# Performance work log

Hardware: AMD Instinct MI355X
Metric: run time of the kernel (lower is better)

## Reference

```python
import jax, jax.numpy as jnp
import numpy as np

N = 100000      # nodes
E = 1600000     # directed edges (avg degree 16)
F_IN = 512      # config.input_layer
H1, D1 = 8, 8   # conv1: 8 heads x 8 dims
C_OUT = 40      # config.output_layer


def setup_inputs() -> dict:
    key = jax.random.key(0)
    ks = jax.random.split(key, 10)
    x = jax.random.normal(ks[0], (N, F_IN), dtype=jnp.float32)
    edge_index = jax.random.randint(ks[1], (2, E), 0, N, dtype=jnp.int64)
    s = 0.05
    W1 = jax.random.normal(ks[2], (F_IN, H1 * D1), dtype=jnp.float32) * s
    att_src1 = jax.random.normal(ks[3], (H1, D1), dtype=jnp.float32) * s
    att_dst1 = jax.random.normal(ks[4], (H1, D1), dtype=jnp.float32) * s
    b1 = jnp.zeros((H1 * D1,), dtype=jnp.float32)
    W2 = jax.random.normal(ks[5], (H1 * D1, C_OUT), dtype=jnp.float32) * s
    att_src2 = jax.random.normal(ks[6], (1, C_OUT), dtype=jnp.float32) * s
    att_dst2 = jax.random.normal(ks[7], (1, C_OUT), dtype=jnp.float32) * s
    b2 = jnp.zeros((C_OUT,), dtype=jnp.float32)
    return {"x": x, "edge_index": edge_index,
            "W1": W1, "att_src1": att_src1, "att_dst1": att_dst1, "b1": b1,
            "W2": W2, "att_src2": att_src2, "att_dst2": att_dst2, "b2": b2}


def _gat_conv(x, src, dst, W, a_src, a_dst, b, heads, concat):
    """PyG GATConv (eval mode: attention dropout is identity)."""
    n = x.shape[0]
    d = W.shape[1] // heads
    h = (x @ W).reshape(n, heads, d)                       # [N,H,D]
    alpha_s = jnp.einsum('nhd,hd->nh', h, a_src)           # [N,H]
    alpha_d = jnp.einsum('nhd,hd->nh', h, a_dst)
    e = jax.nn.leaky_relu(alpha_s[src] + alpha_d[dst], 0.2)  # [E,H]
    # numerically stable segment softmax over edges grouped by dst
    e = e - jax.ops.segment_max(e, dst, num_segments=n)[dst]
    ex = jnp.exp(e)
    denom = jax.ops.segment_sum(ex, dst, num_segments=n)[dst]
    alpha = ex / denom                                      # [E,H]
    msg = h[src] * alpha[:, :, None]                        # [E,H,D]
    out = jax.ops.segment_sum(msg, dst, num_segments=n)     # [N,H,D]
    out = out.reshape(n, heads * d) if concat else out.mean(axis=1)
    return out + b


def reference(x, edge_index, W1, att_src1, att_dst1, b1, W2, att_src2, att_dst2, b2):
    # add self loops (PyG GATConv default)
    loop = jnp.arange(x.shape[0], dtype=edge_index.dtype)
    src = jnp.concatenate([edge_index[0], loop])
    dst = jnp.concatenate([edge_index[1], loop])
    # dropout(p=0.6) layers are identity in eval mode
    h = jax.nn.elu(_gat_conv(x, src, dst, W1, att_src1, att_dst1, b1, H1, True))
    out = _gat_conv(h, src, dst, W2, att_src2, att_dst2, b2, 1, False)
    return jax.nn.log_softmax(out, axis=1)
```

## Files before the change

### kernel.cpp

```cpp
#include <hip/hip_runtime.h>

#define F_IN 512
#define H1   8
#define D1   8
#define C1   64
#define C2   40
#define C2P  48

#define BKT_SH   7
#define BKT_W    128
#define NBKT_MAX 1024
#define NBLK     128

using short8 = __attribute__((ext_vector_type(8))) short;
using f32x4  = __attribute__((ext_vector_type(4))) float;
using bf8v   = __attribute__((ext_vector_type(8))) __bf16;

__device__ __forceinline__ float leaky02(float x) { return x > 0.f ? x : 0.2f * x; }
__device__ __forceinline__ float bf2f(unsigned short u) {
    return __builtin_bit_cast(float, ((unsigned)u) << 16);
}
__device__ __forceinline__ unsigned short f2bf(float v) {
    return __builtin_bit_cast(unsigned short, (__bf16)v);
}
__device__ __forceinline__ short8 cvt_bf16x8(float4 a, float4 b) {
    bf8v r;
    r[0] = (__bf16)a.x; r[1] = (__bf16)a.y; r[2] = (__bf16)a.z; r[3] = (__bf16)a.w;
    r[4] = (__bf16)b.x; r[5] = (__bf16)b.y; r[6] = (__bf16)b.z; r[7] = (__bf16)b.w;
    return __builtin_bit_cast(short8, r);
}

__global__ __launch_bounds__(256) void wconv_kernel(
    const float* __restrict__ W1, const float* __restrict__ W2,
    unsigned short* __restrict__ Bt1, unsigned short* __restrict__ Bt2)
{
    int idx = blockIdx.x * 256 + threadIdx.x;
    if (idx < F_IN * C1) {
        int k = idx >> 6, c = idx & 63;
        Bt1[(size_t)c * F_IN + k] = f2bf(W1[idx]);
    } else if (idx < F_IN * C1 + C2P * 64) {
        int j = idx - F_IN * C1;
        int c = j >> 6, k = j & 63;
        float v = (c < C2) ? W2[k * C2 + c] : 0.f;
        Bt2[c * 64 + k] = f2bf(v);
    }
}

__global__ __launch_bounds__(256) void gemm1_kernel(
    const float* __restrict__ x, const unsigned short* __restrict__ Bt1,
    const float* __restrict__ a_src, const float* __restrict__ a_dst,
    unsigned short* __restrict__ h1b, float* __restrict__ as1,
    float* __restrict__ ad1, int N)
{
    const int tid  = threadIdx.x;
    const int w    = tid >> 6;
    const int lane = tid & 63;
    const int lo   = lane & 15;
    const int kg   = lane >> 4;
    const int n0   = blockIdx.x * 128 + w * 32;

    const int nA = min(n0 + lo, N - 1);
    const int nB = min(n0 + 16 + lo, N - 1);
    const float* xA = x + (size_t)nA * F_IN + kg * 8;
    const float* xB = x + (size_t)nB * F_IN + kg * 8;
    const unsigned short* bp = Bt1 + (size_t)lo * F_IN + kg * 8;

    float a_s[4], a_d[4];
    #pragma unroll
    for (int nt = 0; nt < 4; ++nt) {
        a_s[nt] = a_src[nt * 16 + lo];
        a_d[nt] = a_dst[nt * 16 + lo];
    }

    f32x4 acc[2][4];
    #pragma unroll
    for (int mt = 0; mt < 2; ++mt)
        #pragma unroll
        for (int nt = 0; nt < 4; ++nt)
            acc[mt][nt] = (f32x4){0.f, 0.f, 0.f, 0.f};

    #pragma unroll 4
    for (int s = 0; s < 16; ++s) {
        const int kb = s * 32;
        float4 a0 = *(const float4*)(xA + kb);
        float4 a1 = *(const float4*)(xA + kb + 4);
        float4 c0 = *(const float4*)(xB + kb);
        float4 c1 = *(const float4*)(xB + kb + 4);
        short8 bF[4];
        #pragma unroll
        for (int nt = 0; nt < 4; ++nt)
            bF[nt] = *(const short8*)(bp + (size_t)nt * 16 * F_IN + kb);
        short8 aF0 = cvt_bf16x8(a0, a1);
        short8 aF1 = cvt_bf16x8(c0, c1);
        #pragma unroll
        for (int nt = 0; nt < 4; ++nt) {
            acc[0][nt] = __builtin_amdgcn_mfma_f32_16x16x32_bf16(aF0, bF[nt], acc[0][nt], 0, 0, 0);
            acc[1][nt] = __builtin_amdgcn_mfma_f32_16x16x32_bf16(aF1, bF[nt], acc[1][nt], 0, 0, 0);
        }
    }

    #pragma unroll
    for (int mt = 0; mt < 2; ++mt) {
        #pragma unroll
        for (int j = 0; j < 4; ++j) {
            const int n = n0 + mt * 16 + kg * 4 + j;
            float sv[4], dv[4];
            #pragma unroll
            for (int nt = 0; nt < 4; ++nt) {
                float v = acc[mt][nt][j];
                sv[nt] = v * a_s[nt];
                dv[nt] = v * a_d[nt];
            }
            #pragma unroll
            for (int m = 1; m < 8; m <<= 1) {
                #pragma unroll
                for (int nt = 0; nt < 4; ++nt) {
                    sv[nt] += __shfl_xor(sv[nt], m);
                    dv[nt] += __shfl_xor(dv[nt], m);
                }
            }
            if (n < N) {
                #pragma unroll
                for (int nt = 0; nt < 4; ++nt)
                    h1b[(size_t)n * C1 + nt * 16 + lo] = f2bf(acc[mt][nt][j]);
                if ((lane & 7) == 0) {
                    const int h0 = (lane >> 3) & 1;
                    #pragma unroll
                    for (int nt = 0; nt < 4; ++nt) {
                        as1[n * H1 + h0 + nt * 2] = sv[nt];
                        ad1[n * H1 + h0 + nt * 2] = dv[nt];
                    }
                }
            }
        }
    }
}

__global__ __launch_bounds__(256) void bhist_kernel(
    const int* __restrict__ ei, int* __restrict__ blockhist,
    int E, int nbkt, int chunk)
{
    __shared__ int lh[NBKT_MAX];
    for (int i = threadIdx.x; i < nbkt; i += 256) lh[i] = 0;
    __syncthreads();
    const int b = blockIdx.x;
    const int beg = b * chunk;
    const int end = min(E, beg + chunk);
    for (int e = beg + threadIdx.x; e < end; e += 256)
        atomicAdd(&lh[ei[E + e] >> BKT_SH], 1);
    __syncthreads();
    for (int k = threadIdx.x; k < nbkt; k += 256)
        blockhist[k * NBLK + b] = lh[k];
}

__global__ __launch_bounds__(512) void scan1_kernel(
    const int* __restrict__ in, int* __restrict__ excl,
    int* __restrict__ bsum, int M)
{
    __shared__ int sA[512], sB[512];
    const int t = threadIdx.x;
    const int i = blockIdx.x * 512 + t;
    int v = (i < M) ? in[i] : 0;
    sA[t] = v; __syncthreads();
    int* pin = sA; int* pout = sB;
    #pragma unroll
    for (int off = 1; off < 512; off <<= 1) {
        pout[t] = pin[t] + ((t >= off) ? pin[t - off] : 0);
        __syncthreads();
        int* tmp = pin; pin = pout; pout = tmp;
    }
    if (i < M) excl[i] = pin[t] - v;
    if (t == 511) bsum[blockIdx.x] = pin[511];
}

__global__ __launch_bounds__(256) void scan2_kernel(
    int* __restrict__ bsum, int* __restrict__ bsumo, int NB)
{
    __shared__ int sA[256], sB[256];
    const int t = threadIdx.x;
    int v = (t < NB) ? bsum[t] : 0;
    sA[t] = v; __syncthreads();
    int* pin = sA; int* pout = sB;
    #pragma unroll
    for (int off = 1; off < 256; off <<= 1) {
        pout[t] = pin[t] + ((t >= off) ? pin[t - off] : 0);
        __syncthreads();
        int* tmp = pin; pin = pout; pout = tmp;
    }
    if (t < NB) bsumo[t] = pin[t] - v;
}

__global__ __launch_bounds__(256) void bpart_kernel(
    const int* __restrict__ ei, const int* __restrict__ boffs,
    const int* __restrict__ bsumo, int* __restrict__ ebuf,
    int E, int nbkt, int chunk)
{
    __shared__ int cur[NBKT_MAX];
    const int b = blockIdx.x;
    for (int k = threadIdx.x; k < nbkt; k += 256) {
        const int idx = k * NBLK + b;
        cur[k] = boffs[idx] + bsumo[idx >> 9];
    }
    __syncthreads();
    const int beg = b * chunk;
    const int end = min(E, beg + chunk);
    for (int e = beg + threadIdx.x; e < end; e += 256) {
        int src = ei[e], dst = ei[E + e];
        int pos = atomicAdd(&cur[dst >> BKT_SH], 1);
        ebuf[pos] = (src << BKT_SH) | (dst & (BKT_W - 1));
    }
}

__global__ __launch_bounds__(256) void bsort_kernel(
    const int* __restrict__ boffs, const int* __restrict__ bsumo,
    const int* __restrict__ ebuf, int* __restrict__ rowptr,
    int* __restrict__ esrc, int N, int E, int nbkt)
{
    const int b = blockIdx.x;
    const int tid = threadIdx.x;
    const int i0 = b * NBLK;
    const int base = boffs[i0] + bsumo[i0 >> 9];
    int nxt;
    if (b == nbkt - 1) nxt = E;
    else {
        const int i1 = (b + 1) * NBLK;
        nxt = boffs[i1] + bsumo[i1 >> 9];
    }
    const int cnt = nxt - base;

    __shared__ int hist[BKT_W], scn[BKT_W], cur[BKT_W];
    if (tid < BKT_W) hist[tid] = 0;
    __syncthreads();
    for (int i = tid; i < cnt; i += 256)
        atomicAdd(&hist[ebuf[base + i] & (BKT_W - 1)], 1);
    __syncthreads();
    if (tid < BKT_W) scn[tid] = hist[tid];
    __syncthreads();
    #pragma unroll
    for (int off = 1; off < BKT_W; off <<= 1) {
        int add = 0;
        if (tid < BKT_W && tid >= off) add = scn[tid - off];
        __syncthreads();
        if (tid < BKT_W) scn[tid] += add;
        __syncthreads();
    }
    if (tid < BKT_W) {
        int ex = base + scn[tid] - hist[tid];
        cur[tid] = ex;
        int n0 = b * BKT_W + tid;
        if (n0 < N) rowptr[n0] = ex;
    }
    if (b == 0 && tid == 0) rowptr[N] = E;
    __syncthreads();
    for (int i = tid; i < cnt; i += 256) {
        int p = ebuf[base + i];
        int pos = atomicAdd(&cur[p & (BKT_W - 1)], 1);
        esrc[pos] = (unsigned)p >> BKT_SH;
    }
}

__global__ __launch_bounds__(256) void agg1_kernel(
    const int* __restrict__ rowptr, const int* __restrict__ esrc,
    const unsigned short* __restrict__ h1b, const float* __restrict__ as1,
    const float* __restrict__ ad1, const float* __restrict__ b1,
    unsigned short* __restrict__ h1f, int N)
{
    const int n = blockIdx.x * 4 + (threadIdx.x >> 6);
    if (n >= N) return;
    const int lane = threadIdx.x & 63;
    const int h = lane >> 3;
    const float adh = ad1[n * H1 + h];

    float acc = 0.f, den = 0.f;
    int i = rowptr[n];
    const int end = rowptr[n + 1];
    int s0, s1, s2, s3;
    if (i + 4 <= end) { s0 = esrc[i]; s1 = esrc[i+1]; s2 = esrc[i+2]; s3 = esrc[i+3]; }
    for (; i + 4 <= end; ) {
        const float v0 = bf2f(h1b[(size_t)s0 * C1 + lane]);
        const float v1 = bf2f(h1b[(size_t)s1 * C1 + lane]);
        const float v2 = bf2f(h1b[(size_t)s2 * C1 + lane]);
        const float v3 = bf2f(h1b[(size_t)s3 * C1 + lane]);
        const float a0 = as1[s0 * H1 + h], a1 = as1[s1 * H1 + h];
        const float a2 = as1[s2 * H1 + h], a3 = as1[s3 * H1 + h];
        i += 4;
        const int t0 = esrc[i], t1 = esrc[i+1], t2 = esrc[i+2], t3 = esrc[i+3];
        const float e0 = __expf(leaky02(a0 + adh));
        const float e1 = __expf(leaky02(a1 + adh));
        const float e2 = __expf(leaky02(a2 + adh));
        const float e3 = __expf(leaky02(a3 + adh));
        acc += e0 * v0; acc += e1 * v1; acc += e2 * v2; acc += e3 * v3;
        den += (e0 + e1) + (e2 + e3);
        s0 = t0; s1 = t1; s2 = t2; s3 = t3;
    }
    for (; i < end; ++i) {
        const int src = esrc[i];
        const float v  = bf2f(h1b[(size_t)src * C1 + lane]);
        const float ex = __expf(leaky02(as1[src * H1 + h] + adh));
        acc += ex * v;
        den += ex;
    }
    {
        const float ex = __expf(leaky02(as1[n * H1 + h] + adh));
        acc += ex * bf2f(h1b[(size_t)n * C1 + lane]);
        den += ex;
    }
    float v = acc / den + b1[lane];
    v = v > 0.f ? v : __expf(v) - 1.f;
    h1f[(size_t)n * C1 + lane] = f2bf(v);
}

__global__ __launch_bounds__(256) void gemm2_kernel(
    const unsigned short* __restrict__ h1f, const unsigned short* __restrict__ Bt2,
    const float* __restrict__ a_src2, const float* __restrict__ a_dst2,
    unsigned short* __restrict__ h2b, float* __restrict__ as2,
    float* __restrict__ ad2, int N)
{
    const int tid  = threadIdx.x;
    const int w    = tid >> 6;
    const int lane = tid & 63;
    const int lo   = lane & 15;
    const int kg   = lane >> 4;
    const int n0   = blockIdx.x * 64 + w * 16;

    const int nA = min(n0 + lo, N - 1);
    const unsigned short* ap = h1f + (size_t)nA * C1 + kg * 8;

    float a_s[3], a_d[3];
    #pragma unroll
    for (int nt = 0; nt < 3; ++nt) {
        const int c = nt * 16 + lo;
        a_s[nt] = (c < C2) ? a_src2[c] : 0.f;
        a_d[nt] = (c < C2) ? a_dst2[c] : 0.f;
    }

    f32x4 acc[3];
    #pragma unroll
    for (int nt = 0; nt < 3; ++nt) acc[nt] = (f32x4){0.f, 0.f, 0.f, 0.f};

    #pragma unroll
    for (int ks = 0; ks < 2; ++ks) {
        short8 aF = *(const short8*)(ap + ks * 32);
        #pragma unroll
        for (int nt = 0; nt < 3; ++nt) {
            short8 bF = *(const short8*)(Bt2 + (nt * 16 + lo) * 64 + ks * 32 + kg * 8);
            acc[nt] = __builtin_amdgcn_mfma_f32_16x16x32_bf16(aF, bF, acc[nt], 0, 0, 0);
        }
    }

    #pragma unroll
    for (int j = 0; j < 4; ++j) {
        const int n = n0 + kg * 4 + j;
        float s = acc[0][j] * a_s[0] + acc[1][j] * a_s[1] + acc[2][j] * a_s[2];
        float d = acc[0][j] * a_d[0] + acc[1][j] * a_d[1] + acc[2][j] * a_d[2];
        #pragma unroll
        for (int m = 1; m < 16; m <<= 1) {
            s += __shfl_xor(s, m);
            d += __shfl_xor(d, m);
        }
        if (n < N) {
            #pragma unroll
            for (int nt = 0; nt < 3; ++nt) {
                const int c = nt * 16 + lo;
                if (c < C2) h2b[(size_t)n * C2 + c] = f2bf(acc[nt][j]);
            }
            if (lo == 0) { as2[n] = s; ad2[n] = d; }
        }
    }
}

__global__ __launch_bounds__(256) void agg2_kernel(
    const int* __restrict__ rowptr, const int* __restrict__ esrc,
    const unsigned short* __restrict__ h2b, const float* __restrict__ as2,
    const float* __restrict__ ad2, const float* __restrict__ b2,
    float* __restrict__ out, int N)
{
    const int n = blockIdx.x * 4 + (threadIdx.x >> 6);
    if (n >= N) return;
    const int lane = threadIdx.x & 63;
    const float adn = ad2[n];

    float acc = 0.f, den = 0.f;
    int i = rowptr[n];
    const int end = rowptr[n + 1];
    int s0, s1, s2, s3;
    if (i + 4 <= end) { s0 = esrc[i]; s1 = esrc[i+1]; s2 = esrc[i+2]; s3 = esrc[i+3]; }
    for (; i + 4 <= end; ) {
        float v0 = 0.f, v1 = 0.f, v2 = 0.f, v3 = 0.f;
        if (lane < C2) {
            v0 = bf2f(h2b[(size_t)s0 * C2 + lane]);
            v1 = bf2f(h2b[(size_t)s1 * C2 + lane]);
            v2 = bf2f(h2b[(size_t)s2 * C2 + lane]);
            v3 = bf2f(h2b[(size_t)s3 * C2 + lane]);
        }
        const float a0 = as2[s0], a1 = as2[s1], a2 = as2[s2], a3 = as2[s3];
        i += 4;
        const int t0 = esrc[i], t1 = esrc[i+1], t2 = esrc[i+2], t3 = esrc[i+3];
        const float e0 = __expf(leaky02(a0 + adn));
        const float e1 = __expf(leaky02(a1 + adn));
        const float e2 = __expf(leaky02(a2 + adn));
        const float e3 = __expf(leaky02(a3 + adn));
        acc += e0 * v0; acc += e1 * v1; acc += e2 * v2; acc += e3 * v3;
        den += (e0 + e1) + (e2 + e3);
        s0 = t0; s1 = t1; s2 = t2; s3 = t3;
    }
    for (; i < end; ++i) {
        const int src = esrc[i];
        float v = (lane < C2) ? bf2f(h2b[(size_t)src * C2 + lane]) : 0.f;
        const float ex = __expf(leaky02(as2[src] + adn));
        acc += ex * v;
        den += ex;
    }
    {
        const float ex = __expf(leaky02(as2[n] + adn));
        if (lane < C2) acc += ex * bf2f(h2b[(size_t)n * C2 + lane]);
        den += ex;
    }
    float v = (lane < C2) ? (acc / den + b2[lane]) : -1e30f;
    float m = v;
    #pragma unroll
    for (int s = 1; s < 64; s <<= 1) m = fmaxf(m, __shfl_xor(m, s));
    float e2x = (lane < C2) ? __expf(v - m) : 0.f;
    #pragma unroll
    for (int s = 1; s < 64; s <<= 1) e2x += __shfl_xor(e2x, s);
    float lse = __logf(e2x);
    if (lane < C2) out[(size_t)n * C2 + lane] = v - m - lse;
}

extern "C" void kernel_launch(void* const* d_in, const int* in_sizes, int n_in,
                              void* d_out, int out_size, void* d_ws, size_t ws_size,
                              hipStream_t stream)
{
    const float* x    = (const float*)d_in[0];
    const int*   ei   = (const int*)  d_in[1];
    const float* W1   = (const float*)d_in[2];
    const float* as1w = (const float*)d_in[3];
    const float* ad1w = (const float*)d_in[4];
    const float* b1   = (const float*)d_in[5];
    const float* W2   = (const float*)d_in[6];
    const float* as2w = (const float*)d_in[7];
    const float* ad2w = (const float*)d_in[8];
    const float* b2   = (const float*)d_in[9];

    const int N = in_sizes[0] / F_IN;
    const int E = in_sizes[1] / 2;
    const int nbkt = (N + BKT_W - 1) >> BKT_SH;
    const int M    = nbkt * NBLK;
    const int chunk = (E + NBLK - 1) / NBLK;

    char* base = (char*)d_ws;
    auto carve = [&](size_t bytes) -> void* {
        void* p = (void*)base;
        base += (bytes + 255) & ~(size_t)255;
        return p;
    };
    unsigned short* h1b = (unsigned short*)carve((size_t)N * C1 * 2);
    unsigned short* h1f = (unsigned short*)carve((size_t)N * C1 * 2);
    float* as1    = (float*)carve((size_t)N * H1 * 4);
    float* ad1    = (float*)carve((size_t)N * H1 * 4);
    unsigned short* h2b = (unsigned short*)carve((size_t)N * C2 * 2);
    float* as2    = (float*)carve((size_t)N * 4);
    float* ad2    = (float*)carve((size_t)N * 4);
    int*   rowptr = (int*)carve((size_t)(N + 1) * 4);
    int*   esrc   = (int*)carve((size_t)E * 4);
    int*   boffs  = (int*)carve((size_t)(M + 1) * 4);
    int*   bsum   = (int*)carve(256 * 4);
    int*   bsumo  = (int*)carve(256 * 4);
    unsigned short* Bt1 = (unsigned short*)carve((size_t)F_IN * C1 * 2);
    unsigned short* Bt2 = (unsigned short*)carve((size_t)C2P * 64 * 2);

    int* ebuf = (int*)h1f;

    const int NB = (M + 511) / 512;

    wconv_kernel<<<(F_IN * C1 + C2P * 64 + 255) / 256, 256, 0, stream>>>(W1, W2, Bt1, Bt2);

    bhist_kernel<<<NBLK, 256, 0, stream>>>(ei, boffs, E, nbkt, chunk);
    scan1_kernel<<<NB, 512, 0, stream>>>(boffs, boffs, bsum, M);
    scan2_kernel<<<1, 256, 0, stream>>>(bsum, bsumo, NB);
    bpart_kernel<<<NBLK, 256, 0, stream>>>(ei, boffs, bsumo, ebuf, E, nbkt, chunk);
    bsort_kernel<<<nbkt, 256, 0, stream>>>(boffs, bsumo, ebuf, rowptr, esrc, N, E, nbkt);

    gemm1_kernel<<<(N + 127) / 128, 256, 0, stream>>>(x, Bt1, as1w, ad1w, h1b, as1, ad1, N);
    agg1_kernel<<<(N + 3) / 4, 256, 0, stream>>>(rowptr, esrc, h1b, as1, ad1, b1, h1f, N);
    gemm2_kernel<<<(N + 63) / 64, 256, 0, stream>>>(h1f, Bt2, as2w, ad2w, h2b, as2, ad2, N);
    agg2_kernel<<<(N + 3) / 4, 256, 0, stream>>>(rowptr, esrc, h2b, as2, ad2, b2,
                                                 (float*)d_out, N);
}
```

Baseline: 334.7 us.

## Fuse layer-2 projection into agg1 epilogue and merge histogram into gemm1 launch

```diff
diff --git a/kernel.cpp b/kernel.cpp
--- a/kernel.cpp
+++ b/kernel.cpp
@@ -5,7 +5,6 @@
 #define D1   8
 #define C1   64
 #define C2   40
-#define C2P  48
 
 #define BKT_SH   7
 #define BKT_W    128
@@ -31,33 +30,45 @@
 }
 
 __global__ __launch_bounds__(256) void wconv_kernel(
-    const float* __restrict__ W1, const float* __restrict__ W2,
-    unsigned short* __restrict__ Bt1, unsigned short* __restrict__ Bt2)
+    const float* __restrict__ W1, unsigned short* __restrict__ Bt1)
 {
     int idx = blockIdx.x * 256 + threadIdx.x;
-    if (idx < F_IN * C1) {
-        int k = idx >> 6, c = idx & 63;
-        Bt1[(size_t)c * F_IN + k] = f2bf(W1[idx]);
-    } else if (idx < F_IN * C1 + C2P * 64) {
-        int j = idx - F_IN * C1;
-        int c = j >> 6, k = j & 63;
-        float v = (c < C2) ? W2[k * C2 + c] : 0.f;
-        Bt2[c * 64 + k] = f2bf(v);
-    }
-}
-
-__global__ __launch_bounds__(256) void gemm1_kernel(
+    if (idx >= F_IN * C1) return;
+    int k = idx >> 6, c = idx & 63;
+    Bt1[(size_t)c * F_IN + k] = f2bf(W1[idx]);
+}
+
+__global__ __launch_bounds__(256) void fused1_kernel(
     const float* __restrict__ x, const unsigned short* __restrict__ Bt1,
     const float* __restrict__ a_src, const float* __restrict__ a_dst,
     unsigned short* __restrict__ h1b, float* __restrict__ as1,
-    float* __restrict__ ad1, int N)
-{
-    const int tid  = threadIdx.x;
+    float* __restrict__ ad1, int N,
+    const int* __restrict__ ei, int* __restrict__ blockhist,
+    int E, int nbkt, int chunk, int G1)
+{
+    __shared__ int lh[NBKT_MAX];
+    const int blk = blockIdx.x;
+    const int tid = threadIdx.x;
+
+    if (blk >= G1) {
+        const int b = blk - G1;
+        for (int i = tid; i < nbkt; i += 256) lh[i] = 0;
+        __syncthreads();
+        const int beg = b * chunk;
+        const int end = min(E, beg + chunk);
+        for (int e = beg + tid; e < end; e += 256)
+            atomicAdd(&lh[ei[E + e] >> BKT_SH], 1);
+        __syncthreads();
+        for (int k = tid; k < nbkt; k += 256)
+            blockhist[k * NBLK + b] = lh[k];
+        return;
+    }
+
     const int w    = tid >> 6;
     const int lane = tid & 63;
     const int lo   = lane & 15;
     const int kg   = lane >> 4;
-    const int n0   = blockIdx.x * 128 + w * 32;
+    const int n0   = blk * 128 + w * 32;
 
     const int nA = min(n0 + lo, N - 1);
     const int nB = min(n0 + 16 + lo, N - 1);
@@ -136,23 +147,6 @@
     }
 }
 
-__global__ __launch_bounds__(256) void bhist_kernel(
-    const int* __restrict__ ei, int* __restrict__ blockhist,
-    int E, int nbkt, int chunk)
-{
-    __shared__ int lh[NBKT_MAX];
-    for (int i = threadIdx.x; i < nbkt; i += 256) lh[i] = 0;
-    __syncthreads();
-    const int b = blockIdx.x;
-    const int beg = b * chunk;
-    const int end = min(E, beg + chunk);
-    for (int e = beg + threadIdx.x; e < end; e += 256)
-        atomicAdd(&lh[ei[E + e] >> BKT_SH], 1);
-    __syncthreads();
-    for (int k = threadIdx.x; k < nbkt; k += 256)
-        blockhist[k * NBLK + b] = lh[k];
-}
-
 __global__ __launch_bounds__(512) void scan1_kernel(
     const int* __restrict__ in, int* __restrict__ excl,
     int* __restrict__ bsum, int M)
@@ -263,11 +257,20 @@
     const int* __restrict__ rowptr, const int* __restrict__ esrc,
     const unsigned short* __restrict__ h1b, const float* __restrict__ as1,
     const float* __restrict__ ad1, const float* __restrict__ b1,
-    unsigned short* __restrict__ h1f, int N)
-{
-    const int n = blockIdx.x * 4 + (threadIdx.x >> 6);
+    const float* __restrict__ W2, const float* __restrict__ as2w,
+    const float* __restrict__ ad2w, unsigned short* __restrict__ h2b,
+    float* __restrict__ as2, float* __restrict__ ad2, int N)
+{
+    __shared__ float W2s[C1 * C2];
+    __shared__ float a2sL[C2], a2dL[C2];
+    const int tid = threadIdx.x;
+    for (int i = tid; i < C1 * C2; i += 256) W2s[i] = W2[i];
+    if (tid < C2) { a2sL[tid] = as2w[tid]; a2dL[tid] = ad2w[tid]; }
+    __syncthreads();
+
+    const int n = blockIdx.x * 4 + (tid >> 6);
     if (n >= N) return;
-    const int lane = threadIdx.x & 63;
+    const int lane = tid & 63;
     const int h = lane >> 3;
     const float adh = ad1[n * H1 + h];
 
@@ -307,66 +310,23 @@
     }
     float v = acc / den + b1[lane];
     v = v > 0.f ? v : __expf(v) - 1.f;
-    h1f[(size_t)n * C1 + lane] = f2bf(v);
-}
-
-__global__ __launch_bounds__(256) void gemm2_kernel(
-    const unsigned short* __restrict__ h1f, const unsigned short* __restrict__ Bt2,
-    const float* __restrict__ a_src2, const float* __restrict__ a_dst2,
-    unsigned short* __restrict__ h2b, float* __restrict__ as2,
-    float* __restrict__ ad2, int N)
-{
-    const int tid  = threadIdx.x;
-    const int w    = tid >> 6;
-    const int lane = tid & 63;
-    const int lo   = lane & 15;
-    const int kg   = lane >> 4;
-    const int n0   = blockIdx.x * 64 + w * 16;
-
-    const int nA = min(n0 + lo, N - 1);
-    const unsigned short* ap = h1f + (size_t)nA * C1 + kg * 8;
-
-    float a_s[3], a_d[3];
-    #pragma unroll
-    for (int nt = 0; nt < 3; ++nt) {
-        const int c = nt * 16 + lo;
-        a_s[nt] = (c < C2) ? a_src2[c] : 0.f;
-        a_d[nt] = (c < C2) ? a_dst2[c] : 0.f;
-    }
-
-    f32x4 acc[3];
-    #pragma unroll
-    for (int nt = 0; nt < 3; ++nt) acc[nt] = (f32x4){0.f, 0.f, 0.f, 0.f};
-
-    #pragma unroll
-    for (int ks = 0; ks < 2; ++ks) {
-        short8 aF = *(const short8*)(ap + ks * 32);
-        #pragma unroll
-        for (int nt = 0; nt < 3; ++nt) {
-            short8 bF = *(const short8*)(Bt2 + (nt * 16 + lo) * 64 + ks * 32 + kg * 8);
-            acc[nt] = __builtin_amdgcn_mfma_f32_16x16x32_bf16(aF, bF, acc[nt], 0, 0, 0);
-        }
-    }
-
-    #pragma unroll
-    for (int j = 0; j < 4; ++j) {
-        const int n = n0 + kg * 4 + j;
-        float s = acc[0][j] * a_s[0] + acc[1][j] * a_s[1] + acc[2][j] * a_s[2];
-        float d = acc[0][j] * a_d[0] + acc[1][j] * a_d[1] + acc[2][j] * a_d[2];
-        #pragma unroll
-        for (int m = 1; m < 16; m <<= 1) {
-            s += __shfl_xor(s, m);
-            d += __shfl_xor(d, m);
-        }
-        if (n < N) {
-            #pragma unroll
-            for (int nt = 0; nt < 3; ++nt) {
-                const int c = nt * 16 + lo;
-                if (c < C2) h2b[(size_t)n * C2 + c] = f2bf(acc[nt][j]);
-            }
-            if (lo == 0) { as2[n] = s; ad2[n] = d; }
-        }
-    }
+
+    float acc2 = 0.f;
+    #pragma unroll 8
+    for (int k = 0; k < C1; ++k) {
+        const float hk = __shfl(v, k);
+        const float w = (lane < C2) ? W2s[k * C2 + lane] : 0.f;
+        acc2 += hk * w;
+    }
+    float s2v = (lane < C2) ? acc2 * a2sL[lane] : 0.f;
+    float d2v = (lane < C2) ? acc2 * a2dL[lane] : 0.f;
+    #pragma unroll
+    for (int m = 1; m < 64; m <<= 1) {
+        s2v += __shfl_xor(s2v, m);
+        d2v += __shfl_xor(d2v, m);
+    }
+    if (lane < C2) h2b[(size_t)n * C2 + lane] = f2bf(acc2);
+    if (lane == 0) { as2[n] = s2v; ad2[n] = d2v; }
 }
 
 __global__ __launch_bounds__(256) void agg2_kernel(
@@ -447,6 +407,7 @@
     const int nbkt = (N + BKT_W - 1) >> BKT_SH;
     const int M    = nbkt * NBLK;
     const int chunk = (E + NBLK - 1) / NBLK;
+    const int G1   = (N + 127) / 128;
 
     char* base = (char*)d_ws;
     auto carve = [&](size_t bytes) -> void* {
@@ -455,7 +416,6 @@
         return p;
     };
     unsigned short* h1b = (unsigned short*)carve((size_t)N * C1 * 2);
-    unsigned short* h1f = (unsigned short*)carve((size_t)N * C1 * 2);
     float* as1    = (float*)carve((size_t)N * H1 * 4);
     float* ad1    = (float*)carve((size_t)N * H1 * 4);
     unsigned short* h2b = (unsigned short*)carve((size_t)N * C2 * 2);
@@ -467,23 +427,23 @@
     int*   bsum   = (int*)carve(256 * 4);
     int*   bsumo  = (int*)carve(256 * 4);
     unsigned short* Bt1 = (unsigned short*)carve((size_t)F_IN * C1 * 2);
-    unsigned short* Bt2 = (unsigned short*)carve((size_t)C2P * 64 * 2);
-
-    int* ebuf = (int*)h1f;
+
+    int* ebuf = (int*)h2b;
 
     const int NB = (M + 511) / 512;
 
-    wconv_kernel<<<(F_IN * C1 + C2P * 64 + 255) / 256, 256, 0, stream>>>(W1, W2, Bt1, Bt2);
-
-    bhist_kernel<<<NBLK, 256, 0, stream>>>(ei, boffs, E, nbkt, chunk);
+    wconv_kernel<<<(F_IN * C1 + 255) / 256, 256, 0, stream>>>(W1, Bt1);
+
+    fused1_kernel<<<G1 + NBLK, 256, 0, stream>>>(
+        x, Bt1, as1w, ad1w, h1b, as1, ad1, N, ei, boffs, E, nbkt, chunk, G1);
+
     scan1_kernel<<<NB, 512, 0, stream>>>(boffs, boffs, bsum, M);
     scan2_kernel<<<1, 256, 0, stream>>>(bsum, bsumo, NB);
     bpart_kernel<<<NBLK, 256, 0, stream>>>(ei, boffs, bsumo, ebuf, E, nbkt, chunk);
     bsort_kernel<<<nbkt, 256, 0, stream>>>(boffs, bsumo, ebuf, rowptr, esrc, N, E, nbkt);
 
-    gemm1_kernel<<<(N + 127) / 128, 256, 0, stream>>>(x, Bt1, as1w, ad1w, h1b, as1, ad1, N);
-    agg1_kernel<<<(N + 3) / 4, 256, 0, stream>>>(rowptr, esrc, h1b, as1, ad1, b1, h1f, N);
-    gemm2_kernel<<<(N + 63) / 64, 256, 0, stream>>>(h1f, Bt2, as2w, ad2w, h2b, as2, ad2, N);
+    agg1_kernel<<<(N + 3) / 4, 256, 0, stream>>>(
+        rowptr, esrc, h1b, as1, ad1, b1, W2, as2w, ad2w, h2b, as2, ad2, N);
     agg2_kernel<<<(N + 3) / 4, 256, 0, stream>>>(rowptr, esrc, h2b, as2, ad2, b2,
                                                  (float*)d_out, N);
 }
```

Result: slower. 380.3 us (+13.6%).

## Fuse layer-1 GEMM with edge histogram in one launch; drop index prefetch in aggregation

Applied to the files above, without the earlier changes.

```diff
diff --git a/kernel.cpp b/kernel.cpp
--- a/kernel.cpp
+++ b/kernel.cpp
@@ -46,18 +46,37 @@
     }
 }
 
-__global__ __launch_bounds__(256) void gemm1_kernel(
+__global__ __launch_bounds__(256) void fused1_kernel(
     const float* __restrict__ x, const unsigned short* __restrict__ Bt1,
     const float* __restrict__ a_src, const float* __restrict__ a_dst,
     unsigned short* __restrict__ h1b, float* __restrict__ as1,
-    float* __restrict__ ad1, int N)
-{
-    const int tid  = threadIdx.x;
+    float* __restrict__ ad1, int N,
+    const int* __restrict__ ei, int* __restrict__ blockhist,
+    int E, int nbkt, int chunk, int G1)
+{
+    __shared__ int lh[NBKT_MAX];
+    const int blk = blockIdx.x;
+    const int tid = threadIdx.x;
+
+    if (blk >= G1) {
+        const int b = blk - G1;
+        for (int i = tid; i < nbkt; i += 256) lh[i] = 0;
+        __syncthreads();
+        const int beg = b * chunk;
+        const int end = min(E, beg + chunk);
+        for (int e = beg + tid; e < end; e += 256)
+            atomicAdd(&lh[ei[E + e] >> BKT_SH], 1);
+        __syncthreads();
+        for (int k = tid; k < nbkt; k += 256)
+            blockhist[k * NBLK + b] = lh[k];
+        return;
+    }
+
     const int w    = tid >> 6;
     const int lane = tid & 63;
     const int lo   = lane & 15;
     const int kg   = lane >> 4;
-    const int n0   = blockIdx.x * 128 + w * 32;
+    const int n0   = blk * 128 + w * 32;
 
     const int nA = min(n0 + lo, N - 1);
     const int nB = min(n0 + 16 + lo, N - 1);
@@ -136,23 +155,6 @@
     }
 }
 
-__global__ __launch_bounds__(256) void bhist_kernel(
-    const int* __restrict__ ei, int* __restrict__ blockhist,
-    int E, int nbkt, int chunk)
-{
-    __shared__ int lh[NBKT_MAX];
-    for (int i = threadIdx.x; i < nbkt; i += 256) lh[i] = 0;
-    __syncthreads();
-    const int b = blockIdx.x;
-    const int beg = b * chunk;
-    const int end = min(E, beg + chunk);
-    for (int e = beg + threadIdx.x; e < end; e += 256)
-        atomicAdd(&lh[ei[E + e] >> BKT_SH], 1);
-    __syncthreads();
-    for (int k = threadIdx.x; k < nbkt; k += 256)
-        blockhist[k * NBLK + b] = lh[k];
-}
-
 __global__ __launch_bounds__(512) void scan1_kernel(
     const int* __restrict__ in, int* __restrict__ excl,
     int* __restrict__ bsum, int M)
@@ -274,24 +276,20 @@
     float acc = 0.f, den = 0.f;
     int i = rowptr[n];
     const int end = rowptr[n + 1];
-    int s0, s1, s2, s3;
-    if (i + 4 <= end) { s0 = esrc[i]; s1 = esrc[i+1]; s2 = esrc[i+2]; s3 = esrc[i+3]; }
-    for (; i + 4 <= end; ) {
+    for (; i + 4 <= end; i += 4) {
+        const int s0 = esrc[i], s1 = esrc[i + 1], s2 = esrc[i + 2], s3 = esrc[i + 3];
         const float v0 = bf2f(h1b[(size_t)s0 * C1 + lane]);
         const float v1 = bf2f(h1b[(size_t)s1 * C1 + lane]);
         const float v2 = bf2f(h1b[(size_t)s2 * C1 + lane]);
         const float v3 = bf2f(h1b[(size_t)s3 * C1 + lane]);
         const float a0 = as1[s0 * H1 + h], a1 = as1[s1 * H1 + h];
         const float a2 = as1[s2 * H1 + h], a3 = as1[s3 * H1 + h];
-        i += 4;
-        const int t0 = esrc[i], t1 = esrc[i+1], t2 = esrc[i+2], t3 = esrc[i+3];
         const float e0 = __expf(leaky02(a0 + adh));
         const float e1 = __expf(leaky02(a1 + adh));
         const float e2 = __expf(leaky02(a2 + adh));
         const float e3 = __expf(leaky02(a3 + adh));
         acc += e0 * v0; acc += e1 * v1; acc += e2 * v2; acc += e3 * v3;
         den += (e0 + e1) + (e2 + e3);
-        s0 = t0; s1 = t1; s2 = t2; s3 = t3;
     }
     for (; i < end; ++i) {
         const int src = esrc[i];
@@ -383,9 +381,8 @@
     float acc = 0.f, den = 0.f;
     int i = rowptr[n];
     const int end = rowptr[n + 1];
-    int s0, s1, s2, s3;
-    if (i + 4 <= end) { s0 = esrc[i]; s1 = esrc[i+1]; s2 = esrc[i+2]; s3 = esrc[i+3]; }
-    for (; i + 4 <= end; ) {
+    for (; i + 4 <= end; i += 4) {
+        const int s0 = esrc[i], s1 = esrc[i + 1], s2 = esrc[i + 2], s3 = esrc[i + 3];
         float v0 = 0.f, v1 = 0.f, v2 = 0.f, v3 = 0.f;
         if (lane < C2) {
             v0 = bf2f(h2b[(size_t)s0 * C2 + lane]);
@@ -394,15 +391,12 @@
             v3 = bf2f(h2b[(size_t)s3 * C2 + lane]);
         }
         const float a0 = as2[s0], a1 = as2[s1], a2 = as2[s2], a3 = as2[s3];
-        i += 4;
-        const int t0 = esrc[i], t1 = esrc[i+1], t2 = esrc[i+2], t3 = esrc[i+3];
         const float e0 = __expf(leaky02(a0 + adn));
         const float e1 = __expf(leaky02(a1 + adn));
         const float e2 = __expf(leaky02(a2 + adn));
         const float e3 = __expf(leaky02(a3 + adn));
         acc += e0 * v0; acc += e1 * v1; acc += e2 * v2; acc += e3 * v3;
         den += (e0 + e1) + (e2 + e3);
-        s0 = t0; s1 = t1; s2 = t2; s3 = t3;
     }
     for (; i < end; ++i) {
         const int src = esrc[i];
@@ -447,6 +441,7 @@
     const int nbkt = (N + BKT_W - 1) >> BKT_SH;
     const int M    = nbkt * NBLK;
     const int chunk = (E + NBLK - 1) / NBLK;
+    const int G1   = (N + 127) / 128;
 
     char* base = (char*)d_ws;
     auto carve = [&](size_t bytes) -> void* {
@@ -475,13 +470,14 @@
 
     wconv_kernel<<<(F_IN * C1 + C2P * 64 + 255) / 256, 256, 0, stream>>>(W1, W2, Bt1, Bt2);
 
-    bhist_kernel<<<NBLK, 256, 0, stream>>>(ei, boffs, E, nbkt, chunk);
+    fused1_kernel<<<G1 + NBLK, 256, 0, stream>>>(
+        x, Bt1, as1w, ad1w, h1b, as1, ad1, N, ei, boffs, E, nbkt, chunk, G1);
+
     scan1_kernel<<<NB, 512, 0, stream>>>(boffs, boffs, bsum, M);
     scan2_kernel<<<1, 256, 0, stream>>>(bsum, bsumo, NB);
     bpart_kernel<<<NBLK, 256, 0, stream>>>(ei, boffs, bsumo, ebuf, E, nbkt, chunk);
     bsort_kernel<<<nbkt, 256, 0, stream>>>(boffs, bsumo, ebuf, rowptr, esrc, N, E, nbkt);
 
-    gemm1_kernel<<<(N + 127) / 128, 256, 0, stream>>>(x, Bt1, as1w, ad1w, h1b, as1, ad1, N);
     agg1_kernel<<<(N + 3) / 4, 256, 0, stream>>>(rowptr, esrc, h1b, as1, ad1, b1, h1f, N);
     gemm2_kernel<<<(N + 63) / 64, 256, 0, stream>>>(h1f, Bt2, as2w, ad2w, h2b, as2, ad2, N);
     agg2_kernel<<<(N + 3) / 4, 256, 0, stream>>>(rowptr, esrc, h2b, as2, ad2, b2,
```

Result: faster. 313.0 us (median of 2 runs) (-6.5%).
